# Kernel tuning notes

Hardware: AMD Instinct MI355X
Metric: run time of the kernel (lower is better)

## Reference

```python
import jax, jax.numpy as jnp
import numpy as np

EPS = 1e-5

def setup_inputs() -> dict:
    key = jax.random.key(0)
    ks = jax.random.split(key, 8)
    B, s, i, c = 1, 256, 256, 256
    h, d = 8, 32  # n_head, c_h; h*d == c
    m = jax.random.normal(ks[0], (B, s, i, c), dtype=jnp.float32)
    msa_mask = jnp.ones((B, s, i), dtype=jnp.float32)
    sc = 1.0 / np.sqrt(c)
    return {
        "m": m,
        "msa_mask": msa_mask,
        "ln_w": jnp.ones((c,), jnp.float32),
        "ln_b": jnp.zeros((c,), jnp.float32),
        "wq": jax.random.normal(ks[1], (h * d, c), jnp.float32) * sc,
        "wk": jax.random.normal(ks[2], (h * d, c), jnp.float32) * sc,
        "wv": jax.random.normal(ks[3], (h * d, c), jnp.float32) * sc,
        "wg": jax.random.normal(ks[4], (h * d, c), jnp.float32) * sc,
        "bg": jnp.zeros((h * d,), jnp.float32),
        "wo": jax.random.normal(ks[5], (c, h * d), jnp.float32) * sc,
        "bo": jnp.zeros((c,), jnp.float32),
    }

def _to_heads(x, B, s, i, h, d):
    # [B,s,i,h*d] -> [B,i,h,s,d]
    return jnp.transpose(x.reshape(B, s, i, h, d), (0, 2, 3, 1, 4))

def reference(m, msa_mask, ln_w, ln_b, wq, wk, wv, wg, bg, wo, bo):
    B, s, i, c = m.shape
    hd = wq.shape[0]
    d = 32
    h = hd // d
    # LayerNorm over channel dim
    mu = jnp.mean(m, axis=-1, keepdims=True)
    var = jnp.mean(jnp.square(m - mu), axis=-1, keepdims=True)
    m_norm = (m - mu) * jax.lax.rsqrt(var + EPS) * ln_w + ln_b
    q = _to_heads(m_norm @ wq.T, B, s, i, h, d)
    k = _to_heads(m_norm @ wk.T, B, s, i, h, d)
    v = _to_heads(m_norm @ wv.T, B, s, i, h, d)
    gate = jax.nn.sigmoid(_to_heads(m_norm @ wg.T + bg, B, s, i, h, d))
    # masks: msa_mask [B,s,i] -> keys mask [B,i,s]
    mk = jnp.transpose(msa_mask, (0, 2, 1)) > 0
    mv = mk.astype(q.dtype)[:, :, None, :, None]  # [B,i,1,s,1]
    q = q * mv
    k = k * mv
    v = v * mv
    gate = gate * mv
    # attention over sequence dim s (per column i)
    logits = jnp.einsum('bihqd,bihkd->bihqk', q, k) / jnp.sqrt(jnp.asarray(d, q.dtype))
    pair_mask = (mk[:, :, None, :] & mk[:, :, :, None])[:, :, None, :, :]  # [B,i,1,s,s]
    logits = jnp.where(pair_mask, logits, jnp.asarray(-1e9, q.dtype))
    attn = jax.nn.softmax(logits, axis=-1)
    o = jnp.einsum('bihqk,bihkd->bihqd', attn, v)
    o = o * gate * mv
    # [B,i,h,s,d] -> [B,i,s,h*d]
    o = jnp.transpose(o, (0, 1, 3, 2, 4)).reshape(B, i, s, h * d)
    o = o @ wo.T + bo  # [B,i,s,c]
    return jnp.transpose(o, (0, 2, 1, 3))  # [B,s,i,c]
```

## Files before the change

kernel.cpp:

```cpp
#include <hip/hip_runtime.h>

typedef unsigned short u16;
typedef unsigned int u32;
typedef __attribute__((ext_vector_type(8))) short short8;
typedef __attribute__((ext_vector_type(4))) float f32x4;

constexpr int S_ = 256, I_ = 256, C_ = 256, H_ = 8, D_ = 32, HD_ = 256;
constexpr float QSCALE = 0.17677669529663687f;

__device__ __forceinline__ float b2f(u32 u) {
  union { u32 i; float f; } x; x.i = u << 16; return x.f;
}
__device__ __forceinline__ u16 f2b(float f) {
  union { float f; u32 i; } x; x.f = f;
  u32 r = x.i + 0x7fffu + ((x.i >> 16) & 1u);
  return (u16)(r >> 16);
}
__device__ __forceinline__ uint4 pack8(const float* f) {
  uint4 r;
  r.x = (u32)f2b(f[0]) | ((u32)f2b(f[1]) << 16);
  r.y = (u32)f2b(f[2]) | ((u32)f2b(f[3]) << 16);
  r.z = (u32)f2b(f[4]) | ((u32)f2b(f[5]) << 16);
  r.w = (u32)f2b(f[6]) | ((u32)f2b(f[7]) << 16);
  return r;
}
__device__ __forceinline__ void load8f(const float* p, float* f) {
  float4 a = *reinterpret_cast<const float4*>(p);
  float4 b = *reinterpret_cast<const float4*>(p + 4);
  f[0] = a.x; f[1] = a.y; f[2] = a.z; f[3] = a.w;
  f[4] = b.x; f[5] = b.y; f[6] = b.z; f[7] = b.w;
}
__device__ __forceinline__ f32x4 mfma16(short8 a, short8 b, f32x4 c) {
  return __builtin_amdgcn_mfma_f32_16x16x32_bf16(a, b, c, 0, 0, 0);
}

__global__ void k_lnnorm(const float* __restrict__ m, const float* __restrict__ mask,
                         const float* __restrict__ lnw, const float* __restrict__ lnb,
                         u16* __restrict__ mn) {
  int wg = (blockIdx.x * 256 + threadIdx.x) >> 6;
  int lane = threadIdx.x & 63;
  float4 wv = *reinterpret_cast<const float4*>(lnw + lane * 4);
  float4 bv = *reinterpret_cast<const float4*>(lnb + lane * 4);
  for (int it = 0; it < 8; ++it) {
    int row = wg * 8 + it;
    float4 v = *reinterpret_cast<const float4*>(m + (size_t)row * C_ + lane * 4);
    float s = v.x + v.y + v.z + v.w;
    float ss = v.x * v.x + v.y * v.y + v.z * v.z + v.w * v.w;
#pragma unroll
    for (int o = 32; o; o >>= 1) { s += __shfl_xor(s, o); ss += __shfl_xor(ss, o); }
    float mean = s * (1.f / C_);
    float var = ss * (1.f / C_) - mean * mean;
    float rs = rsqrtf(fmaxf(var, 0.f) + 1e-5f);
    float mk = mask[row];
    float y[4];
    y[0] = ((v.x - mean) * rs * wv.x + bv.x) * mk;
    y[1] = ((v.y - mean) * rs * wv.y + bv.y) * mk;
    y[2] = ((v.z - mean) * rs * wv.z + bv.z) * mk;
    y[3] = ((v.w - mean) * rs * wv.w + bv.w) * mk;
    uint2 pk;
    pk.x = (u32)f2b(y[0]) | ((u32)f2b(y[1]) << 16);
    pk.y = (u32)f2b(y[2]) | ((u32)f2b(y[3]) << 16);
    *reinterpret_cast<uint2*>(mn + (size_t)row * C_ + lane * 4) = pk;
  }
}

__global__ void k_wpack(const float* __restrict__ wq, const float* __restrict__ wk,
                        const float* __restrict__ wv, const float* __restrict__ wg,
                        const float* __restrict__ wo, u16* __restrict__ wall2) {
  int gid = blockIdx.x * 4 + (threadIdx.x >> 6);
  int lane = threadIdx.x & 63;
  if (gid >= 640) return;
  const float* W;
  int g2;
  if (gid < 512) {
    int mat = gid >> 7;
    W = (mat == 0) ? wq : (mat == 1) ? wk : (mat == 2) ? wv : wg;
    g2 = gid & 127;
  } else {
    W = wo;
    g2 = gid - 512;
  }
  int nn = g2 & 1, kk = (g2 >> 1) & 7, ch2 = (g2 >> 4) & 1, cbi = (g2 >> 5) & 3;
  int row = cbi * 64 + ch2 * 32 + nn * 16 + (lane & 15);
  int k0 = kk * 32 + (lane >> 4) * 8;
  float f[8];
  load8f(W + (size_t)row * 256 + k0, f);
  *reinterpret_cast<uint4*>(wall2 + (size_t)gid * 512 + lane * 8) = pack8(f);
}

__global__ __launch_bounds__(256, 4) void k_qkvg(
    const u16* __restrict__ mn, const float* __restrict__ mask,
    const u16* __restrict__ wall2, const float* __restrict__ bg,
    u16* __restrict__ qws, u16* __restrict__ kws, u16* __restrict__ vws,
    u16* __restrict__ gws) {
  __shared__ u16 lA[64 * 256];
  int tile = blockIdx.x;
  int i_col = tile >> 2, s0 = (tile & 3) * 64;
  int t = threadIdx.x;
  int rowg = t >> 5, cg = t & 31;
#pragma unroll
  for (int p = 0; p < 8; ++p) {
    int row = p * 8 + rowg;
    int rg = (s0 + row) * I_ + i_col;
    *reinterpret_cast<uint4*>(&lA[row * 256 + ((cg * 8) ^ ((row & 7) << 3))]) =
        *reinterpret_cast<const uint4*>(mn + (size_t)rg * C_ + cg * 8);
  }
  __syncthreads();
  int lane = t & 63, w = t >> 6;
  int wr = (w >> 1) * 32, ch2 = w & 1, wc = ch2 * 32;
  int lr = lane & 15, lk = lane >> 4;
  f32x4 zz = {0.f, 0.f, 0.f, 0.f};
  for (int chunk = 0; chunk < 16; ++chunk) {
    int mat = chunk >> 2, cb = (chunk & 3) * 64;
    const u16* Bp = wall2 + (size_t)((chunk * 2 + ch2) * 16) * 512 + lane * 8;
    f32x4 acc[2][2] = {{zz, zz}, {zz, zz}};
#pragma unroll
    for (int kk = 0; kk < 8; ++kk) {
      int kb = kk * 32 + lk * 8;
      int ra0 = wr + lr, ra1 = wr + 16 + lr;
      short8 a0 = *reinterpret_cast<const short8*>(&lA[ra0 * 256 + (kb ^ ((ra0 & 7) << 3))]);
      short8 a1 = *reinterpret_cast<const short8*>(&lA[ra1 * 256 + (kb ^ ((ra1 & 7) << 3))]);
      short8 b0 = *reinterpret_cast<const short8*>(Bp + (kk * 2 + 0) * 512);
      short8 b1 = *reinterpret_cast<const short8*>(Bp + (kk * 2 + 1) * 512);
      acc[0][0] = mfma16(a0, b0, acc[0][0]);
      acc[0][1] = mfma16(a0, b1, acc[0][1]);
      acc[1][0] = mfma16(a1, b0, acc[1][0]);
      acc[1][1] = mfma16(a1, b1, acc[1][1]);
    }
#pragma unroll
    for (int mm = 0; mm < 2; ++mm) {
#pragma unroll
      for (int nn = 0; nn < 2; ++nn) {
        int colL = wc + nn * 16 + lr;
        int hd = cb + colL;
        int h = hd >> 5, d = hd & 31;
        if (mat == 2) {
          int sbase = s0 + wr + mm * 16 + lk * 4;
          uint2 pk;
          pk.x = (u32)f2b(acc[mm][nn][0]) | ((u32)f2b(acc[mm][nn][1]) << 16);
          pk.y = (u32)f2b(acc[mm][nn][2]) | ((u32)f2b(acc[mm][nn][3]) << 16);
          *reinterpret_cast<uint2*>(
              vws + (((size_t)i_col * H_ + h) * D_ + d) * S_ + sbase) = pk;
        } else {
          u16* dstp = (mat == 0) ? qws : (mat == 1) ? kws : gws;
          float bgv = (mat == 3) ? bg[hd] : 0.f;
#pragma unroll
          for (int r = 0; r < 4; ++r) {
            int rowL = wr + mm * 16 + lk * 4 + r;
            int s = s0 + rowL;
            float v = acc[mm][nn][r];
            if (mat == 0) v *= QSCALE;
            if (mat == 3) {
              float mkv = mask[s * I_ + i_col];
              v = mkv * (1.f / (1.f + __expf(-(v + bgv))));
            }
            dstp[(((size_t)i_col * H_ + h) * S_ + s) * D_ + d] = f2b(v);
          }
        }
      }
    }
  }
}

__global__ __launch_bounds__(1024) void k_attn(
    u16* __restrict__ qws, const u16* __restrict__ kws,
    const u16* __restrict__ vws, const u16* __restrict__ gws,
    const float* __restrict__ mask) {
  __shared__ u16 lK[256 * 40];
  __shared__ u16 lV[32 * 264];
  __shared__ float lMk[256];
  int bid = blockIdx.x;
  int i = bid >> 3, h = bid & 7;
  int t = threadIdx.x;
  size_t base = ((size_t)i * H_ + h) * (size_t)(S_ * D_);
  {
    int s = t >> 2, part = t & 3;
    *reinterpret_cast<uint4*>(&lK[s * 40 + part * 8]) =
        *reinterpret_cast<const uint4*>(kws + base + s * 32 + part * 8);
    int d = t >> 5, p2 = t & 31;
    *reinterpret_cast<uint4*>(&lV[d * 264 + p2 * 8]) =
        *reinterpret_cast<const uint4*>(vws + base + d * 256 + p2 * 8);
    if (t < 256) lMk[t] = mask[t * I_ + i];
  }
  __syncthreads();
  int lane = t & 63;
  int wvid = t >> 6;
  int lq = lane & 15, g = lane >> 4;
  int qbase = wvid * 16;
  short8 qf = *reinterpret_cast<const short8*>(qws + base + (size_t)(qbase + lq) * D_ + g * 8);
  f32x4 zz = {0.f, 0.f, 0.f, 0.f};
  f32x4 o0 = zz, o1 = zz;
  float mcur = -1e30f, sumd = 0.f;
  int addrP0 = (lq + ((g & 1) * 2 + 0) * 16) * 4;
  int addrP1 = (lq + ((g & 1) * 2 + 1) * 16) * 4;
  int aC0 = (g * 4 + 0) * 4, aC1 = (g * 4 + 1) * 4;
  int aC2 = (g * 4 + 2) * 4, aC3 = (g * 4 + 3) * 4;
#pragma unroll
  for (int ks = 0; ks < 8; ++ks) {
    int k0 = ks * 32;
    short8 kf0 = *reinterpret_cast<const short8*>(&lK[(k0 + lq) * 40 + g * 8]);
    short8 kf1 = *reinterpret_cast<const short8*>(&lK[(k0 + 16 + lq) * 40 + g * 8]);
    f32x4 s0 = mfma16(kf0, qf, zz);
    f32x4 s1 = mfma16(kf1, qf, zz);
    float4 mk0 = *reinterpret_cast<const float4*>(&lMk[k0 + g * 4]);
    float4 mk1 = *reinterpret_cast<const float4*>(&lMk[k0 + 16 + g * 4]);
    float sv[8];
    sv[0] = mk0.x > 0.f ? s0[0] : -1e9f;
    sv[1] = mk0.y > 0.f ? s0[1] : -1e9f;
    sv[2] = mk0.z > 0.f ? s0[2] : -1e9f;
    sv[3] = mk0.w > 0.f ? s0[3] : -1e9f;
    sv[4] = mk1.x > 0.f ? s1[0] : -1e9f;
    sv[5] = mk1.y > 0.f ? s1[1] : -1e9f;
    sv[6] = mk1.z > 0.f ? s1[2] : -1e9f;
    sv[7] = mk1.w > 0.f ? s1[3] : -1e9f;
    float tmax = fmaxf(fmaxf(fmaxf(sv[0], sv[1]), fmaxf(sv[2], sv[3])),
                       fmaxf(fmaxf(sv[4], sv[5]), fmaxf(sv[6], sv[7])));
    tmax = fmaxf(tmax, __shfl_xor(tmax, 16));
    tmax = fmaxf(tmax, __shfl_xor(tmax, 32));
    bool skip = __all(tmax <= mcur + 8.0f);
    if (!skip) {
      float mnew = fmaxf(mcur, tmax);
      float c = __expf(mcur - mnew);
      mcur = mnew;
      sumd *= c;
      float co0 = __int_as_float(__builtin_amdgcn_ds_bpermute(aC0, __float_as_int(c)));
      float co1 = __int_as_float(__builtin_amdgcn_ds_bpermute(aC1, __float_as_int(c)));
      float co2 = __int_as_float(__builtin_amdgcn_ds_bpermute(aC2, __float_as_int(c)));
      float co3 = __int_as_float(__builtin_amdgcn_ds_bpermute(aC3, __float_as_int(c)));
      o0[0] *= co0; o0[1] *= co1; o0[2] *= co2; o0[3] *= co3;
      o1[0] *= co0; o1[1] *= co1; o1[2] *= co2; o1[3] *= co3;
    }
    float p[8];
#pragma unroll
    for (int j = 0; j < 8; ++j) p[j] = __expf(sv[j] - mcur);
    sumd += ((p[0] + p[1]) + (p[2] + p[3])) + ((p[4] + p[5]) + (p[6] + p[7]));
    u32 pk00 = (u32)f2b(p[0]) | ((u32)f2b(p[1]) << 16);
    u32 pk01 = (u32)f2b(p[2]) | ((u32)f2b(p[3]) << 16);
    u32 pk10 = (u32)f2b(p[4]) | ((u32)f2b(p[5]) << 16);
    u32 pk11 = (u32)f2b(p[6]) | ((u32)f2b(p[7]) << 16);
    int b00 = __builtin_amdgcn_ds_bpermute(addrP0, (int)pk00);
    int b10 = __builtin_amdgcn_ds_bpermute(addrP0, (int)pk10);
    int b01 = __builtin_amdgcn_ds_bpermute(addrP0, (int)pk01);
    int b11 = __builtin_amdgcn_ds_bpermute(addrP0, (int)pk11);
    int b02 = __builtin_amdgcn_ds_bpermute(addrP1, (int)pk00);
    int b12 = __builtin_amdgcn_ds_bpermute(addrP1, (int)pk10);
    int b03 = __builtin_amdgcn_ds_bpermute(addrP1, (int)pk01);
    int b13 = __builtin_amdgcn_ds_bpermute(addrP1, (int)pk11);
    union { int u[4]; short8 s8; } pu;
    bool lo = (g < 2);
    pu.u[0] = lo ? b00 : b10;
    pu.u[1] = lo ? b01 : b11;
    pu.u[2] = lo ? b02 : b12;
    pu.u[3] = lo ? b03 : b13;
    short8 vf0 = *reinterpret_cast<const short8*>(&lV[lq * 264 + k0 + g * 8]);
    short8 vf1 = *reinterpret_cast<const short8*>(&lV[(16 + lq) * 264 + k0 + g * 8]);
    o0 = mfma16(pu.s8, vf0, o0);
    o1 = mfma16(pu.s8, vf1, o1);
  }
  float s2 = sumd + __shfl_xor(sumd, 16);
  float tot = s2 + __shfl_xor(s2, 32);
  float iv = 1.f / tot;
  float ivo[4];
  ivo[0] = __int_as_float(__builtin_amdgcn_ds_bpermute(aC0, __float_as_int(iv)));
  ivo[1] = __int_as_float(__builtin_amdgcn_ds_bpermute(aC1, __float_as_int(iv)));
  ivo[2] = __int_as_float(__builtin_amdgcn_ds_bpermute(aC2, __float_as_int(iv)));
  ivo[3] = __int_as_float(__builtin_amdgcn_ds_bpermute(aC3, __float_as_int(iv)));
#pragma unroll
  for (int r = 0; r < 4; ++r) {
    int row = qbase + g * 4 + r;
    size_t idx0 = base + (size_t)row * D_ + lq;
    size_t idx1 = idx0 + 16;
    float g0 = b2f((u32)gws[idx0]);
    float g1 = b2f((u32)gws[idx1]);
    qws[idx0] = f2b(o0[r] * ivo[r] * g0);
    qws[idx1] = f2b(o1[r] * ivo[r] * g1);
  }
}

__global__ __launch_bounds__(512) void k_oproj(const u16* __restrict__ ows,
                                               const u16* __restrict__ wall2,
                                               const float* __restrict__ bo,
                                               float* __restrict__ out) {
  __shared__ u16 lA[64 * 256];
  int tile = blockIdx.x;
  int r0 = tile * 64;
  int t = threadIdx.x;
  int rowg = t >> 5, cg = t & 31;
  int hh = cg >> 2, d0 = (cg & 3) * 8;
#pragma unroll
  for (int p = 0; p < 4; ++p) {
    int row = p * 16 + rowg;
    int rg = r0 + row;
    int ii = rg >> 8, ss = rg & 255;
    *reinterpret_cast<uint4*>(&lA[row * 256 + ((cg * 8) ^ ((row & 7) << 3))]) =
        *reinterpret_cast<const uint4*>(ows + (((size_t)ii * H_ + hh) * S_ + ss) * D_ + d0);
  }
  __syncthreads();
  int lane = t & 63, w = t >> 6;
  int wr = (w >> 2) * 32, ch4 = w & 3;
  int lr = lane & 15, lk = lane >> 4;
  f32x4 zz = {0.f, 0.f, 0.f, 0.f};
  for (int chunk = 0; chunk < 4; ++chunk) {
    int cb = chunk * 64;
    const u16* Bp =
        wall2 + (size_t)(512 + (chunk * 2 + (ch4 >> 1)) * 16 + (ch4 & 1)) * 512 + lane * 8;
    f32x4 acc0 = zz, acc1 = zz;
#pragma unroll
    for (int kk = 0; kk < 8; ++kk) {
      int kb = kk * 32 + lk * 8;
      int ra0 = wr + lr, ra1 = wr + 16 + lr;
      short8 a0 = *reinterpret_cast<const short8*>(&lA[ra0 * 256 + (kb ^ ((ra0 & 7) << 3))]);
      short8 a1 = *reinterpret_cast<const short8*>(&lA[ra1 * 256 + (kb ^ ((ra1 & 7) << 3))]);
      short8 b0 = *reinterpret_cast<const short8*>(Bp + kk * 1024);
      acc0 = mfma16(a0, b0, acc0);
      acc1 = mfma16(a1, b0, acc1);
    }
    int ch = cb + ch4 * 16 + lr;
    float bov = bo[ch];
#pragma unroll
    for (int mm = 0; mm < 2; ++mm) {
      const f32x4& acc = (mm == 0) ? acc0 : acc1;
#pragma unroll
      for (int r = 0; r < 4; ++r) {
        int rg = r0 + wr + mm * 16 + lk * 4 + r;
        int ii = rg >> 8;
        int ss = rg & 255;
        out[((size_t)ss * I_ + ii) * C_ + ch] = acc[r] + bov;
      }
    }
  }
}

extern "C" void kernel_launch(void* const* d_in, const int* in_sizes, int n_in,
                              void* d_out, int out_size, void* d_ws, size_t ws_size,
                              hipStream_t stream) {
  const float *m, *mask, *lnw, *lnb, *wq, *wk, *wv, *wg, *bg, *wo, *bo;
  if (in_sizes[0] > 1000000) {
    m = (const float*)d_in[0]; mask = (const float*)d_in[1];
    lnw = (const float*)d_in[2]; lnb = (const float*)d_in[3];
    wq = (const float*)d_in[4]; wk = (const float*)d_in[5];
    wv = (const float*)d_in[6]; wg = (const float*)d_in[7];
    bg = (const float*)d_in[8]; wo = (const float*)d_in[9];
    bo = (const float*)d_in[10];
  } else {
    bg = (const float*)d_in[0]; bo = (const float*)d_in[1];
    lnb = (const float*)d_in[2]; lnw = (const float*)d_in[3];
    m = (const float*)d_in[4]; mask = (const float*)d_in[5];
    wg = (const float*)d_in[6]; wk = (const float*)d_in[7];
    wo = (const float*)d_in[8]; wq = (const float*)d_in[9];
    wv = (const float*)d_in[10];
  }
  float* out = (float*)d_out;

  const size_t SZ = (size_t)S_ * I_ * C_;
  u16* qws = (u16*)d_ws;
  u16* kws = qws + SZ;
  u16* vws = kws + SZ;
  u16* gws = vws + SZ;
  u16* mn = gws + SZ;
  u16* wall2 = mn + SZ;

  k_lnnorm<<<2048, 256, 0, stream>>>(m, mask, lnw, lnb, mn);
  k_wpack<<<160, 256, 0, stream>>>(wq, wk, wv, wg, wo, wall2);
  k_qkvg<<<1024, 256, 0, stream>>>(mn, mask, wall2, bg, qws, kws, vws, gws);
  k_attn<<<2048, 1024, 0, stream>>>(qws, kws, vws, gws, mask);
  k_oproj<<<1024, 512, 0, stream>>>(qws, wall2, bo, out);
}
```

Baseline: 192.6 us.

## Split QKVG projection across 8 waves by output column block

The projection kernel now runs with 512 threads, with 8 waves. Each wave covers all 64 rows of the tile and one 32-column slice of a 64-column block, looping over the four matrices. Before, each of 4 waves covered 32 rows and looped over all 16 chunks. This doubles the wave parallelism per tile and lets each weight fragment be reused across 4 row blocks instead of 2, which halves global weight loads per MFMA. In exchange it needs more accumulator registers and drops the occupancy hint.

```diff
diff --git a/kernel.cpp b/kernel.cpp
--- a/kernel.cpp
+++ b/kernel.cpp
@@ -88,7 +88,7 @@
   *reinterpret_cast<uint4*>(wall2 + (size_t)gid * 512 + lane * 8) = pack8(f);
 }
 
-__global__ __launch_bounds__(256, 4) void k_qkvg(
+__global__ __launch_bounds__(512) void k_qkvg(
     const u16* __restrict__ mn, const float* __restrict__ mask,
     const u16* __restrict__ wall2, const float* __restrict__ bg,
     u16* __restrict__ qws, u16* __restrict__ kws, u16* __restrict__ vws,
@@ -99,58 +99,61 @@
   int t = threadIdx.x;
   int rowg = t >> 5, cg = t & 31;
 #pragma unroll
-  for (int p = 0; p < 8; ++p) {
-    int row = p * 8 + rowg;
+  for (int p = 0; p < 4; ++p) {
+    int row = p * 16 + rowg;
     int rg = (s0 + row) * I_ + i_col;
     *reinterpret_cast<uint4*>(&lA[row * 256 + ((cg * 8) ^ ((row & 7) << 3))]) =
         *reinterpret_cast<const uint4*>(mn + (size_t)rg * C_ + cg * 8);
   }
   __syncthreads();
   int lane = t & 63, w = t >> 6;
-  int wr = (w >> 1) * 32, ch2 = w & 1, wc = ch2 * 32;
+  int csel = w >> 1;
+  int ch2 = w & 1;
+  int wc = ch2 * 32;
   int lr = lane & 15, lk = lane >> 4;
+  int cb = csel * 64;
   f32x4 zz = {0.f, 0.f, 0.f, 0.f};
-  for (int chunk = 0; chunk < 16; ++chunk) {
-    int mat = chunk >> 2, cb = (chunk & 3) * 64;
+#pragma unroll
+  for (int it = 0; it < 4; ++it) {
+    int chunk = it * 4 + csel;
     const u16* Bp = wall2 + (size_t)((chunk * 2 + ch2) * 16) * 512 + lane * 8;
-    f32x4 acc[2][2] = {{zz, zz}, {zz, zz}};
+    f32x4 acc[4][2] = {{zz, zz}, {zz, zz}, {zz, zz}, {zz, zz}};
 #pragma unroll
     for (int kk = 0; kk < 8; ++kk) {
       int kb = kk * 32 + lk * 8;
-      int ra0 = wr + lr, ra1 = wr + 16 + lr;
-      short8 a0 = *reinterpret_cast<const short8*>(&lA[ra0 * 256 + (kb ^ ((ra0 & 7) << 3))]);
-      short8 a1 = *reinterpret_cast<const short8*>(&lA[ra1 * 256 + (kb ^ ((ra1 & 7) << 3))]);
       short8 b0 = *reinterpret_cast<const short8*>(Bp + (kk * 2 + 0) * 512);
       short8 b1 = *reinterpret_cast<const short8*>(Bp + (kk * 2 + 1) * 512);
-      acc[0][0] = mfma16(a0, b0, acc[0][0]);
-      acc[0][1] = mfma16(a0, b1, acc[0][1]);
-      acc[1][0] = mfma16(a1, b0, acc[1][0]);
-      acc[1][1] = mfma16(a1, b1, acc[1][1]);
-    }
-#pragma unroll
-    for (int mm = 0; mm < 2; ++mm) {
+#pragma unroll
+      for (int mm = 0; mm < 4; ++mm) {
+        int ra = mm * 16 + lr;
+        short8 a = *reinterpret_cast<const short8*>(&lA[ra * 256 + (kb ^ ((ra & 7) << 3))]);
+        acc[mm][0] = mfma16(a, b0, acc[mm][0]);
+        acc[mm][1] = mfma16(a, b1, acc[mm][1]);
+      }
+    }
+#pragma unroll
+    for (int mm = 0; mm < 4; ++mm) {
 #pragma unroll
       for (int nn = 0; nn < 2; ++nn) {
         int colL = wc + nn * 16 + lr;
         int hd = cb + colL;
         int h = hd >> 5, d = hd & 31;
-        if (mat == 2) {
-          int sbase = s0 + wr + mm * 16 + lk * 4;
+        if (it == 2) {
+          int sbase = s0 + mm * 16 + lk * 4;
           uint2 pk;
           pk.x = (u32)f2b(acc[mm][nn][0]) | ((u32)f2b(acc[mm][nn][1]) << 16);
           pk.y = (u32)f2b(acc[mm][nn][2]) | ((u32)f2b(acc[mm][nn][3]) << 16);
           *reinterpret_cast<uint2*>(
               vws + (((size_t)i_col * H_ + h) * D_ + d) * S_ + sbase) = pk;
         } else {
-          u16* dstp = (mat == 0) ? qws : (mat == 1) ? kws : gws;
-          float bgv = (mat == 3) ? bg[hd] : 0.f;
+          u16* dstp = (it == 0) ? qws : (it == 1) ? kws : gws;
+          float bgv = (it == 3) ? bg[hd] : 0.f;
 #pragma unroll
           for (int r = 0; r < 4; ++r) {
-            int rowL = wr + mm * 16 + lk * 4 + r;
-            int s = s0 + rowL;
+            int s = s0 + mm * 16 + lk * 4 + r;
             float v = acc[mm][nn][r];
-            if (mat == 0) v *= QSCALE;
-            if (mat == 3) {
+            if (it == 0) v *= QSCALE;
+            if (it == 3) {
               float mkv = mask[s * I_ + i_col];
               v = mkv * (1.f / (1.f + __expf(-(v + bgv))));
             }
@@ -362,7 +365,7 @@
 
   k_lnnorm<<<2048, 256, 0, stream>>>(m, mask, lnw, lnb, mn);
   k_wpack<<<160, 256, 0, stream>>>(wq, wk, wv, wg, wo, wall2);
-  k_qkvg<<<1024, 256, 0, stream>>>(mn, mask, wall2, bg, qws, kws, vws, gws);
+  k_qkvg<<<1024, 512, 0, stream>>>(mn, mask, wall2, bg, qws, kws, vws, gws);
   k_attn<<<2048, 1024, 0, stream>>>(qws, kws, vws, gws, mask);
   k_oproj<<<1024, 512, 0, stream>>>(qws, wall2, bo, out);
 }
```

Measured after the change: 196.8 us. 1.02x slower.

## Merge prep kernels and store Q and gate transposed for packed stores

Applied to the files above, without the earlier changes.

Merges the layernorm and weight-pack kernels into one launch by splitting on block index. The QKVG projection now writes Q, V and gate in a [d][s] transposed layout using packed 8-byte stores, while K keeps the [s][d] layout. This replaces the scattered 2-byte stores in the epilogue. The attention kernel now gathers Q and gate with strided scalar loads and writes its output to a reused buffer instead of overwriting Q in place, so reads there become less coalesced in exchange for cheaper projection stores.

```diff
diff --git a/kernel.cpp b/kernel.cpp
--- a/kernel.cpp
+++ b/kernel.cpp
@@ -34,65 +34,66 @@
   return __builtin_amdgcn_mfma_f32_16x16x32_bf16(a, b, c, 0, 0, 0);
 }
 
-__global__ void k_lnnorm(const float* __restrict__ m, const float* __restrict__ mask,
-                         const float* __restrict__ lnw, const float* __restrict__ lnb,
-                         u16* __restrict__ mn) {
-  int wg = (blockIdx.x * 256 + threadIdx.x) >> 6;
-  int lane = threadIdx.x & 63;
-  float4 wv = *reinterpret_cast<const float4*>(lnw + lane * 4);
-  float4 bv = *reinterpret_cast<const float4*>(lnb + lane * 4);
-  for (int it = 0; it < 8; ++it) {
-    int row = wg * 8 + it;
-    float4 v = *reinterpret_cast<const float4*>(m + (size_t)row * C_ + lane * 4);
-    float s = v.x + v.y + v.z + v.w;
-    float ss = v.x * v.x + v.y * v.y + v.z * v.z + v.w * v.w;
-#pragma unroll
-    for (int o = 32; o; o >>= 1) { s += __shfl_xor(s, o); ss += __shfl_xor(ss, o); }
-    float mean = s * (1.f / C_);
-    float var = ss * (1.f / C_) - mean * mean;
-    float rs = rsqrtf(fmaxf(var, 0.f) + 1e-5f);
-    float mk = mask[row];
-    float y[4];
-    y[0] = ((v.x - mean) * rs * wv.x + bv.x) * mk;
-    y[1] = ((v.y - mean) * rs * wv.y + bv.y) * mk;
-    y[2] = ((v.z - mean) * rs * wv.z + bv.z) * mk;
-    y[3] = ((v.w - mean) * rs * wv.w + bv.w) * mk;
-    uint2 pk;
-    pk.x = (u32)f2b(y[0]) | ((u32)f2b(y[1]) << 16);
-    pk.y = (u32)f2b(y[2]) | ((u32)f2b(y[3]) << 16);
-    *reinterpret_cast<uint2*>(mn + (size_t)row * C_ + lane * 4) = pk;
-  }
-}
-
-__global__ void k_wpack(const float* __restrict__ wq, const float* __restrict__ wk,
-                        const float* __restrict__ wv, const float* __restrict__ wg,
-                        const float* __restrict__ wo, u16* __restrict__ wall2) {
-  int gid = blockIdx.x * 4 + (threadIdx.x >> 6);
-  int lane = threadIdx.x & 63;
-  if (gid >= 640) return;
-  const float* W;
-  int g2;
-  if (gid < 512) {
-    int mat = gid >> 7;
-    W = (mat == 0) ? wq : (mat == 1) ? wk : (mat == 2) ? wv : wg;
-    g2 = gid & 127;
+__global__ void k_prep(const float* __restrict__ m, const float* __restrict__ mask,
+                       const float* __restrict__ lnw, const float* __restrict__ lnb,
+                       const float* __restrict__ wq, const float* __restrict__ wk,
+                       const float* __restrict__ wv, const float* __restrict__ wg,
+                       const float* __restrict__ wo, u16* __restrict__ mn,
+                       u16* __restrict__ wall2) {
+  if (blockIdx.x < 2048) {
+    int wg = (blockIdx.x * 256 + threadIdx.x) >> 6;
+    int lane = threadIdx.x & 63;
+    float4 wv4 = *reinterpret_cast<const float4*>(lnw + lane * 4);
+    float4 bv4 = *reinterpret_cast<const float4*>(lnb + lane * 4);
+    for (int it = 0; it < 8; ++it) {
+      int row = wg * 8 + it;
+      float4 v = *reinterpret_cast<const float4*>(m + (size_t)row * C_ + lane * 4);
+      float s = v.x + v.y + v.z + v.w;
+      float ss = v.x * v.x + v.y * v.y + v.z * v.z + v.w * v.w;
+#pragma unroll
+      for (int o = 32; o; o >>= 1) { s += __shfl_xor(s, o); ss += __shfl_xor(ss, o); }
+      float mean = s * (1.f / C_);
+      float var = ss * (1.f / C_) - mean * mean;
+      float rs = rsqrtf(fmaxf(var, 0.f) + 1e-5f);
+      float mk = mask[row];
+      float y[4];
+      y[0] = ((v.x - mean) * rs * wv4.x + bv4.x) * mk;
+      y[1] = ((v.y - mean) * rs * wv4.y + bv4.y) * mk;
+      y[2] = ((v.z - mean) * rs * wv4.z + bv4.z) * mk;
+      y[3] = ((v.w - mean) * rs * wv4.w + bv4.w) * mk;
+      uint2 pk;
+      pk.x = (u32)f2b(y[0]) | ((u32)f2b(y[1]) << 16);
+      pk.y = (u32)f2b(y[2]) | ((u32)f2b(y[3]) << 16);
+      *reinterpret_cast<uint2*>(mn + (size_t)row * C_ + lane * 4) = pk;
+    }
   } else {
-    W = wo;
-    g2 = gid - 512;
-  }
-  int nn = g2 & 1, kk = (g2 >> 1) & 7, ch2 = (g2 >> 4) & 1, cbi = (g2 >> 5) & 3;
-  int row = cbi * 64 + ch2 * 32 + nn * 16 + (lane & 15);
-  int k0 = kk * 32 + (lane >> 4) * 8;
-  float f[8];
-  load8f(W + (size_t)row * 256 + k0, f);
-  *reinterpret_cast<uint4*>(wall2 + (size_t)gid * 512 + lane * 8) = pack8(f);
+    int gid = (blockIdx.x - 2048) * 4 + (threadIdx.x >> 6);
+    int lane = threadIdx.x & 63;
+    if (gid >= 640) return;
+    const float* W;
+    int g2;
+    if (gid < 512) {
+      int mat = gid >> 7;
+      W = (mat == 0) ? wq : (mat == 1) ? wk : (mat == 2) ? wv : wg;
+      g2 = gid & 127;
+    } else {
+      W = wo;
+      g2 = gid - 512;
+    }
+    int nn = g2 & 1, kk = (g2 >> 1) & 7, ch2 = (g2 >> 4) & 1, cbi = (g2 >> 5) & 3;
+    int row = cbi * 64 + ch2 * 32 + nn * 16 + (lane & 15);
+    int k0 = kk * 32 + (lane >> 4) * 8;
+    float f[8];
+    load8f(W + (size_t)row * 256 + k0, f);
+    *reinterpret_cast<uint4*>(wall2 + (size_t)gid * 512 + lane * 8) = pack8(f);
+  }
 }
 
 __global__ __launch_bounds__(256, 4) void k_qkvg(
     const u16* __restrict__ mn, const float* __restrict__ mask,
     const u16* __restrict__ wall2, const float* __restrict__ bg,
-    u16* __restrict__ qws, u16* __restrict__ kws, u16* __restrict__ vws,
-    u16* __restrict__ gws) {
+    u16* __restrict__ qT, u16* __restrict__ kws, u16* __restrict__ vT,
+    u16* __restrict__ gT) {
   __shared__ u16 lA[64 * 256];
   int tile = blockIdx.x;
   int i_col = tile >> 2, s0 = (tile & 3) * 64;
@@ -134,28 +135,38 @@
         int colL = wc + nn * 16 + lr;
         int hd = cb + colL;
         int h = hd >> 5, d = hd & 31;
-        if (mat == 2) {
-          int sbase = s0 + wr + mm * 16 + lk * 4;
+        int sbase = s0 + wr + mm * 16 + lk * 4;
+        if (mat == 1) {
+#pragma unroll
+          for (int r = 0; r < 4; ++r) {
+            kws[(((size_t)i_col * H_ + h) * S_ + sbase + r) * D_ + d] =
+                f2b(acc[mm][nn][r]);
+          }
+        } else {
+          float v4[4];
+#pragma unroll
+          for (int r = 0; r < 4; ++r) v4[r] = acc[mm][nn][r];
+          u16* dstp;
+          if (mat == 0) {
+#pragma unroll
+            for (int r = 0; r < 4; ++r) v4[r] *= QSCALE;
+            dstp = qT;
+          } else if (mat == 2) {
+            dstp = vT;
+          } else {
+            float bgv = bg[hd];
+#pragma unroll
+            for (int r = 0; r < 4; ++r) {
+              float mkv = mask[(sbase + r) * I_ + i_col];
+              v4[r] = mkv * (1.f / (1.f + __expf(-(v4[r] + bgv))));
+            }
+            dstp = gT;
+          }
           uint2 pk;
-          pk.x = (u32)f2b(acc[mm][nn][0]) | ((u32)f2b(acc[mm][nn][1]) << 16);
-          pk.y = (u32)f2b(acc[mm][nn][2]) | ((u32)f2b(acc[mm][nn][3]) << 16);
+          pk.x = (u32)f2b(v4[0]) | ((u32)f2b(v4[1]) << 16);
+          pk.y = (u32)f2b(v4[2]) | ((u32)f2b(v4[3]) << 16);
           *reinterpret_cast<uint2*>(
-              vws + (((size_t)i_col * H_ + h) * D_ + d) * S_ + sbase) = pk;
-        } else {
-          u16* dstp = (mat == 0) ? qws : (mat == 1) ? kws : gws;
-          float bgv = (mat == 3) ? bg[hd] : 0.f;
-#pragma unroll
-          for (int r = 0; r < 4; ++r) {
-            int rowL = wr + mm * 16 + lk * 4 + r;
-            int s = s0 + rowL;
-            float v = acc[mm][nn][r];
-            if (mat == 0) v *= QSCALE;
-            if (mat == 3) {
-              float mkv = mask[s * I_ + i_col];
-              v = mkv * (1.f / (1.f + __expf(-(v + bgv))));
-            }
-            dstp[(((size_t)i_col * H_ + h) * S_ + s) * D_ + d] = f2b(v);
-          }
+              dstp + (((size_t)i_col * H_ + h) * D_ + d) * S_ + sbase) = pk;
         }
       }
     }
@@ -163,9 +174,9 @@
 }
 
 __global__ __launch_bounds__(1024) void k_attn(
-    u16* __restrict__ qws, const u16* __restrict__ kws,
-    const u16* __restrict__ vws, const u16* __restrict__ gws,
-    const float* __restrict__ mask) {
+    const u16* __restrict__ qT, const u16* __restrict__ kws,
+    const u16* __restrict__ vT, const u16* __restrict__ gT,
+    const float* __restrict__ mask, u16* __restrict__ ows) {
   __shared__ u16 lK[256 * 40];
   __shared__ u16 lV[32 * 264];
   __shared__ float lMk[256];
@@ -179,7 +190,7 @@
         *reinterpret_cast<const uint4*>(kws + base + s * 32 + part * 8);
     int d = t >> 5, p2 = t & 31;
     *reinterpret_cast<uint4*>(&lV[d * 264 + p2 * 8]) =
-        *reinterpret_cast<const uint4*>(vws + base + d * 256 + p2 * 8);
+        *reinterpret_cast<const uint4*>(vT + base + d * 256 + p2 * 8);
     if (t < 256) lMk[t] = mask[t * I_ + i];
   }
   __syncthreads();
@@ -187,7 +198,13 @@
   int wvid = t >> 6;
   int lq = lane & 15, g = lane >> 4;
   int qbase = wvid * 16;
-  short8 qf = *reinterpret_cast<const short8*>(qws + base + (size_t)(qbase + lq) * D_ + g * 8);
+  short8 qf;
+  {
+    const u16* Q = qT + base;
+    int s = qbase + lq;
+#pragma unroll
+    for (int e = 0; e < 8; ++e) qf[e] = (short)Q[(g * 8 + e) * 256 + s];
+  }
   f32x4 zz = {0.f, 0.f, 0.f, 0.f};
   f32x4 o0 = zz, o1 = zz;
   float mcur = -1e30f, sumd = 0.f;
@@ -268,12 +285,10 @@
 #pragma unroll
   for (int r = 0; r < 4; ++r) {
     int row = qbase + g * 4 + r;
-    size_t idx0 = base + (size_t)row * D_ + lq;
-    size_t idx1 = idx0 + 16;
-    float g0 = b2f((u32)gws[idx0]);
-    float g1 = b2f((u32)gws[idx1]);
-    qws[idx0] = f2b(o0[r] * ivo[r] * g0);
-    qws[idx1] = f2b(o1[r] * ivo[r] * g1);
+    float g0 = b2f((u32)gT[base + (size_t)lq * 256 + row]);
+    float g1 = b2f((u32)gT[base + (size_t)(lq + 16) * 256 + row]);
+    ows[base + (size_t)row * D_ + lq] = f2b(o0[r] * ivo[r] * g0);
+    ows[base + (size_t)row * D_ + lq + 16] = f2b(o1[r] * ivo[r] * g1);
   }
 }
 
@@ -353,16 +368,15 @@
   float* out = (float*)d_out;
 
   const size_t SZ = (size_t)S_ * I_ * C_;
-  u16* qws = (u16*)d_ws;
-  u16* kws = qws + SZ;
-  u16* vws = kws + SZ;
-  u16* gws = vws + SZ;
-  u16* mn = gws + SZ;
+  u16* qT = (u16*)d_ws;
+  u16* kws = qT + SZ;
+  u16* vT = kws + SZ;
+  u16* gT = vT + SZ;
+  u16* mn = gT + SZ;
   u16* wall2 = mn + SZ;
 
-  k_lnnorm<<<2048, 256, 0, stream>>>(m, mask, lnw, lnb, mn);
-  k_wpack<<<160, 256, 0, stream>>>(wq, wk, wv, wg, wo, wall2);
-  k_qkvg<<<1024, 256, 0, stream>>>(mn, mask, wall2, bg, qws, kws, vws, gws);
-  k_attn<<<2048, 1024, 0, stream>>>(qws, kws, vws, gws, mask);
-  k_oproj<<<1024, 512, 0, stream>>>(qws, wall2, bo, out);
-}
+  k_prep<<<2208, 256, 0, stream>>>(m, mask, lnw, lnb, wq, wk, wv, wg, wo, mn, wall2);
+  k_qkvg<<<1024, 256, 0, stream>>>(mn, mask, wall2, bg, qT, kws, vT, gT);
+  k_attn<<<2048, 1024, 0, stream>>>(qT, kws, vT, gT, mask, mn);
+  k_oproj<<<1024, 512, 0, stream>>>(mn, wall2, bo, out);
+}
```

Result: no change. 191.7 us (-0.5%).
